# Kernel tuning notes

Hardware: AMD Instinct MI355X
Metric: run time of the kernel (lower is better)

Reference implementation:

```python
import jax, jax.numpy as jnp
import numpy as np

B, C, H, W = 64, 256, 48, 48
NH = 8          # num_heads
DH = C // NH    # per-head dim = 32
DFF = 2 * C     # FFN hidden = 512 (hard-coded d_ffn=feature_dim*2)
M = 64          # base_class_num
EPS_NORM = 1e-5
EPS_LN = 1e-5


def setup_inputs() -> dict:
    key = jax.random.key(0)
    ks = jax.random.split(key, 12)
    s = 0.02
    return {
        "feature": jax.random.normal(ks[0], (B, C, H, W), jnp.float32),
        "base_class_weight": jax.random.normal(ks[1], (M, C), jnp.float32),
        # 1x1-conv projections (weight [out,in], bias [out])
        "wq": jax.random.normal(ks[2], (C, C), jnp.float32) * s,
        "bq": jnp.zeros((C,), jnp.float32),
        "wk": jax.random.normal(ks[3], (C, C), jnp.float32) * s,
        "bk": jnp.zeros((C,), jnp.float32),
        "wv": jax.random.normal(ks[4], (C, C), jnp.float32) * s,
        "bv": jnp.zeros((C,), jnp.float32),
        "wm": jax.random.normal(ks[5], (C, C), jnp.float32) * s,
        "bm": jnp.zeros((C,), jnp.float32),
        # FFN_MLP
        "w1": jax.random.normal(ks[6], (DFF, C), jnp.float32) * s,
        "b1": jnp.zeros((DFF,), jnp.float32),
        "w2": jax.random.normal(ks[7], (C, DFF), jnp.float32) * s,
        "b2": jnp.zeros((C,), jnp.float32),
        "gamma": jnp.ones((C,), jnp.float32),
        "beta": jnp.zeros((C,), jnp.float32),
    }


def reference(feature, base_class_weight, wq, bq, wk, bk, wv, bv, wm, bm,
              w1, b1, w2, b2, gamma, beta):
    b, c, h, w = feature.shape
    n = h * w
    feat_cn = feature.reshape(b, c, n)                 # [B,c,N]  (q input, channel-first)
    feat_nc = feat_cn.transpose(0, 2, 1)               # [B,N,c]  ('feature' var in torch)
    kv_cm = jnp.broadcast_to(base_class_weight.T[None], (b, c, M))  # [B,c,M]

    # 1x1-conv projections then split channels as [dim, heads] (dim outer, per torch view)
    qp = (jnp.einsum('oc,bcn->bon', wq, feat_cn) + bq[None, :, None]).reshape(b, DH, NH, n)
    kp = (jnp.einsum('oc,bcm->bom', wk, kv_cm) + bk[None, :, None]).reshape(b, DH, NH, M)
    vp = (jnp.einsum('oc,bcm->bom', wv, kv_cm) + bv[None, :, None]).reshape(b, DH, NH, M)

    scores = jnp.einsum('bdhn,bdhm->bhnm', qp, kp) / jnp.sqrt(jnp.float32(DH))
    prob = jax.nn.softmax(scores, axis=-1)             # [B,H,N,M]
    x = jnp.einsum('bhnm,bdhm->bdhn', prob, vp)        # [B,dim,H,N]
    merged = jnp.einsum('oc,bcn->bon', wm, x.reshape(b, c, n)) + bm[None, :, None]  # [B,c,N]

    # SFTA cosine re-weighting
    aligned = merged.transpose(0, 2, 1)                # [B,N,c]
    an = aligned / (jnp.linalg.norm(aligned, axis=-1, keepdims=True) + EPS_NORM)
    fn = feat_nc / (jnp.linalg.norm(feat_nc, axis=-1, keepdims=True) + EPS_NORM)
    cos = jnp.sum(an * fn, axis=-1)                    # [B,N]
    out = feat_nc * (cos + 1.0)[:, :, None]            # [B,N,c]

    # FFN_MLP (dropout = identity in eval) + residual + LayerNorm
    h1 = jax.nn.relu(jnp.einsum('bnc,fc->bnf', out, w1) + b1)
    src2 = jnp.einsum('bnf,cf->bnc', h1, w2) + b2
    src = out + src2
    mu = jnp.mean(src, axis=-1, keepdims=True)
    var = jnp.mean(jnp.square(src - mu), axis=-1, keepdims=True)
    src = (src - mu) / jnp.sqrt(var + EPS_LN) * gamma + beta

    return src.transpose(0, 2, 1).reshape(b, c, h, w)
```

## Files before the change

kernel.cpp:

```cpp
#include <hip/hip_runtime.h>

#define Bc   64
#define Cc   256
#define Nn   2304
#define DFFf 512
#define Mm   64
#define NTILE 64
#define NTB   36

typedef __bf16 bf16_t;
typedef __bf16 bf16x8 __attribute__((ext_vector_type(8)));
typedef __bf16 bf16x4 __attribute__((ext_vector_type(4)));
typedef float  f32x4  __attribute__((ext_vector_type(4)));

__device__ __forceinline__ bf16_t cvt(float f) { return (bf16_t)f; }

__device__ __forceinline__ f32x4 mfma16(bf16x8 a, bf16x8 b, f32x4 c) {
    return __builtin_amdgcn_mfma_f32_16x16x32_bf16(a, b, c, 0, 0, 0);
}

__global__ void kv_kernel(const float* __restrict__ wk, const float* __restrict__ bk,
                          const float* __restrict__ wv, const float* __restrict__ bv,
                          const float* __restrict__ bcw,
                          float* __restrict__ Kout, float* __restrict__ Vout) {
    int c = blockIdx.x;
    int m = threadIdx.x;
    const float* wkr = wk + c * Cc;
    const float* wvr = wv + c * Cc;
    const float* br  = bcw + m * Cc;
    float aK = 0.f, aV = 0.f;
    #pragma unroll 8
    for (int i = 0; i < Cc; ++i) {
        float bcv = br[i];
        aK = fmaf(wkr[i], bcv, aK);
        aV = fmaf(wvr[i], bcv, aV);
    }
    Kout[c * Mm + m] = aK + bk[c];
    Vout[c * Mm + m] = aV + bv[c];
}

__global__ void pack_kernel(const float* __restrict__ wq, const float* __restrict__ bq,
                            const float* __restrict__ wm, const float* __restrict__ w1,
                            const float* __restrict__ w2,
                            const float* __restrict__ Kf32, const float* __restrict__ Vf32,
                            bf16_t* __restrict__ wqf, bf16_t* __restrict__ wmf,
                            bf16_t* __restrict__ w1f, bf16_t* __restrict__ w2f,
// ... 19 lines not shown
        int c = (k & 31) * 8 + (k >> 5);
        wmf[e] = cvt(wm[o * 256 + c]);
    } else if (idx < 262144) {
        int e = idx - 131072;
        int j = e & 7, lane = (e >> 3) & 63, rs = e >> 9;
        int ks = rs & 7, rt = rs >> 3;
        w1f[e] = cvt(w1[(rt * 16 + (lane & 15)) * 256 + ks * 32 + (lane >> 4) * 8 + j]);
    } else if (idx < 393216) {
        int e = idx - 262144;
        int j = e & 7, lane = (e >> 3) & 63, rs = e >> 9;
        int ks = rs & 15, rt = rs >> 4;
        w2f[e] = cvt(w2[(rt * 16 + (lane & 15)) * 512 + ks * 32 + (lane >> 4) * 8 + j]);
    } else if (idx < 409600) {
        int e = idx - 393216;
        int j = e & 7, lane = (e >> 3) & 63, hm = e >> 9;
        int mt = hm & 3, h = hm >> 2;
        int lid = lane & 15;
        int d = (lane >> 4) * 8 + j;
        int m = 32 * (mt >> 1) + 4 * (mt & 1) + 8 * (lid >> 2) + (lid & 3);
        Kf[e] = cvt(Kf32[(d * 8 + h) * 64 + m]);
    } else if (idx < 425984) {
        int e = idx - 409600;
        int j = e & 7, lane = (e >> 3) & 63, x = e >> 9;
        int ks = x & 1, rt = (x >> 1) & 1, h = x >> 2;
        int d = rt * 16 + (lane & 15), m = ks * 32 + (lane >> 4) * 8 + j;
        Vf[e] = cvt(Vf32[(d * 8 + h) * 64 + m]);
    } else if (idx < 426240) {
        int op = idx - 425984;
        int c = (op & 31) * 8 + (op >> 5);
        bqp[op] = bq[c];
    }
}

__global__ __launch_bounds__(512, 4) void sfta_mfma(
    const float* __restrict__ feat,
    const bf16_t* __restrict__ wqf, const float* __restrict__ bqp,
    const bf16_t* __restrict__ wmf, const float* __restrict__ bm,
    const bf16_t* __restrict__ w1f, const float* __restrict__ b1,
    const bf16_t* __restrict__ w2f, const float* __restrict__ b2,
    const bf16_t* __restrict__ Kf,  const bf16_t* __restrict__ Vf,
    const float* __restrict__ gam,  const float* __restrict__ bet,
    float* __restrict__ out) {
    __shared__ __align__(16) bf16_t sFeat[64 * 264];
    __shared__ __align__(16) bf16_t sQX[64 * 264];
    __shared__ float sRed[3][8][64];

    const int t    = threadIdx.x;
    const int wid  = t >> 6;
    const int lane = t & 63;
    const int quad = lane >> 4;
    const int lid  = lane & 15;
    const int b    = blockIdx.y;
    const int n0   = blockIdx.x * NTILE;
    const size_t baseF = (size_t)b * Cc * Nn + n0;

    {
        int cb = t >> 4;
        int nb = (t & 15) * 4;
        #pragma unroll
        for (int i = 0; i < 8; ++i) {
            int c = i * 32 + cb;
            const float4 f4 = *(const float4*)(feat + baseF + (size_t)c * Nn + nb);
            sFeat[(nb + 0) * 264 + c] = cvt(f4.x);
            sFeat[(nb + 1) * 264 + c] = cvt(f4.y);
            sFeat[(nb + 2) * 264 + c] = cvt(f4.z);
            sFeat[(nb + 3) * 264 + c] = cvt(f4.w);
        }
    }
    __syncthreads();

    bf16x8 bq[4];
    {
        f32x4 qacc[2][4];
        #pragma unroll
        for (int rtl = 0; rtl < 2; ++rtl)
            #pragma unroll
            for (int nt = 0; nt < 4; ++nt) qacc[rtl][nt] = (f32x4){0.f, 0.f, 0.f, 0.f};
        #pragma unroll
        for (int ks = 0; ks < 8; ++ks) {
            bf16x8 bfr[4];
            #pragma unroll
            for (int nt = 0; nt < 4; ++nt)
                bfr[nt] = *(const bf16x8*)(sFeat + (nt * 16 + lid) * 264 + ks * 32 + quad * 8);
            #pragma unroll
            for (int rtl = 0; rtl < 2; ++rtl) {
                bf16x8 a = *(const bf16x8*)(wqf + (((wid * 2 + rtl) * 8 + ks) * 64 + lane) * 8);
                #pragma unroll
                for (int nt = 0; nt < 4; ++nt) qacc[rtl][nt] = mfma16(a, bfr[nt], qacc[rtl][nt]);
            }
        }
        const float4 qbA = *(const float4*)(bqp + wid * 32 + quad * 8);
        const float4 qbB = *(const float4*)(bqp + wid * 32 + quad * 8 + 4);
        #pragma unroll
        for (int g = 0; g < 4; ++g) {
            bq[g][0] = cvt(qacc[0][g][0] + qbA.x);
            bq[g][1] = cvt(qacc[0][g][1] + qbA.y);
            bq[g][2] = cvt(qacc[0][g][2] + qbA.z);
            bq[g][3] = cvt(qacc[0][g][3] + qbA.w);
            bq[g][4] = cvt(qacc[1][g][0] + qbB.x);
            bq[g][5] = cvt(qacc[1][g][1] + qbB.y);
            bq[g][6] = cvt(qacc[1][g][2] + qbB.z);
            bq[g][7] = cvt(qacc[1][g][3] + qbB.w);
        }
    }

    {
        bf16x8 kb[4], va[4];
        #pragma unroll
        for (int mt = 0; mt < 4; ++mt)
            kb[mt] = *(const bf16x8*)(Kf + ((wid * 4 + mt) * 64 + lane) * 8);
        #pragma unroll
        for (int rv = 0; rv < 4; ++rv)
            va[rv] = *(const bf16x8*)(Vf + ((wid * 4 + rv) * 64 + lane) * 8);
        const float scl2 = 0.17677669529663687f * 1.4426950408889634f;
        #pragma unroll 1
        for (int g = 0; g < 4; ++g) {
            f32x4 sc[4];
            #pragma unroll
            for (int mt = 0; mt < 4; ++mt) {
                f32x4 z = {0.f, 0.f, 0.f, 0.f};
                sc[mt] = mfma16(kb[mt], bq[g], z);
            }
            float f[16];
            #pragma unroll
            for (int mt = 0; mt < 4; ++mt)
                #pragma unroll
                for (int r = 0; r < 4; ++r) f[mt * 4 + r] = sc[mt][r] * scl2;
            float mx = f[0];
            #pragma unroll
            for (int i = 1; i < 16; ++i) mx = fmaxf(mx, f[i]);
            mx = fmaxf(mx, __shfl_xor(mx, 16));
            mx = fmaxf(mx, __shfl_xor(mx, 32));
            float s = 0.f;
            #pragma unroll
            for (int i = 0; i < 16; ++i) { f[i] = exp2f(f[i] - mx); s += f[i]; }
            s += __shfl_xor(s, 16);
            s += __shfl_xor(s, 32);
            float inv = 1.f / s;
            bf16x8 bp[2];
            #pragma unroll
            for (int ks = 0; ks < 2; ++ks)
                #pragma unroll
                for (int jj = 0; jj < 8; ++jj)
                    bp[ks][jj] = cvt(f[(2 * ks + (jj >> 2)) * 4 + (jj & 3)] * inv);
            #pragma unroll
            for (int rv = 0; rv < 2; ++rv) {
                f32x4 x = {0.f, 0.f, 0.f, 0.f};
                x = mfma16(va[rv * 2 + 0], bp[0], x);
                x = mfma16(va[rv * 2 + 1], bp[1], x);
                bf16x4 o;
                #pragma unroll
                for (int r = 0; r < 4; ++r) o[r] = cvt(x[r]);
                *(bf16x4*)(sQX + (g * 16 + lid) * 264 + wid * 32 + rv * 16 + quad * 4) = o;
            }
        }
    }
    __syncthreads();

    f32x4 acc2[2][4];
    float pmf[4], pmm[4], pff[4];
    {
        #pragma unroll
        for (int rtl = 0; rtl < 2; ++rtl)
            #pragma unroll
            for (int nt = 0; nt < 4; ++nt) acc2[rtl][nt] = (f32x4){0.f, 0.f, 0.f, 0.f};
        #pragma unroll
        for (int ks = 0; ks < 8; ++ks) {
            bf16x8 bx[4];
            #pragma unroll
            for (int nt = 0; nt < 4; ++nt)
                bx[nt] = *(const bf16x8*)(sQX + (nt * 16 + lid) * 264 + ks * 32 + quad * 8);
            #pragma unroll
            for (int rtl = 0; rtl < 2; ++rtl) {
                bf16x8 a = *(const bf16x8*)(wmf + (((wid * 2 + rtl) * 8 + ks) * 64 + lane) * 8);
                #pragma unroll
                for (int nt = 0; nt < 4; ++nt) acc2[rtl][nt] = mfma16(a, bx[nt], acc2[rtl][nt]);
            }
        }
        float4 bmv[2];
        bmv[0] = *(const float4*)(bm + (wid * 2 + 0) * 16 + quad * 4);
        bmv[1] = *(const float4*)(bm + (wid * 2 + 1) * 16 + quad * 4);
        #pragma unroll
        for (int nt = 0; nt < 4; ++nt) { pmf[nt] = 0.f; pmm[nt] = 0.f; pff[nt] = 0.f; }
        #pragma unroll
        for (int rtl = 0; rtl < 2; ++rtl) {
            int ob = (wid * 2 + rtl) * 16 + quad * 4;
            #pragma unroll
            for (int nt = 0; nt < 4; ++nt) {
                bf16x4 f4 = *(const bf16x4*)(sFeat + (nt * 16 + lid) * 264 + ob);
                #pragma unroll
                for (int r = 0; r < 4; ++r) {
                    float m = acc2[rtl][nt][r] + bmv[rtl][r];
                    float f = (float)f4[r];
                    pmf[nt] = fmaf(m, f, pmf[nt]);
                    pmm[nt] = fmaf(m, m, pmm[nt]);
                    pff[nt] = fmaf(f, f, pff[nt]);
                }
            }
        }
    }
    #pragma unroll
    for (int nt = 0; nt < 4; ++nt) {
        pmf[nt] += __shfl_xor(pmf[nt], 16); pmf[nt] += __shfl_xor(pmf[nt], 32);
        pmm[nt] += __shfl_xor(pmm[nt], 16); pmm[nt] += __shfl_xor(pmm[nt], 32);
        pff[nt] += __shfl_xor(pff[nt], 16); pff[nt] += __shfl_xor(pff[nt], 32);
    }
    if (lane < 16) {
        #pragma unroll
        for (int nt = 0; nt < 4; ++nt) {
            sRed[0][wid][nt * 16 + lane] = pmf[nt];
            sRed[1][wid][nt * 16 + lane] = pmm[nt];
            sRed[2][wid][nt * 16 + lane] = pff[nt];
        }
    }
    __syncthreads();

    {
        int row = wid * 8 + (lane >> 3);
        int c0  = (lane & 7) * 32;
        float smf = 0.f, smm = 0.f, sff = 0.f;
        #pragma unroll
        for (int k = 0; k < 8; ++k) {
            smf += sRed[0][k][row];
            smm += sRed[1][k][row];
            sff += sRed[2][k][row];
        }
        float scale = smf / ((sqrtf(smm) + 1e-5f) * (sqrtf(sff) + 1e-5f)) + 1.f;
        bf16_t* frow = sFeat + row * 264 + c0;
        #pragma unroll
        for (int i = 0; i < 4; ++i) {
            bf16x8* pp = (bf16x8*)(frow + i * 8);
            bf16x8 v = *pp;
            #pragma unroll
            for (int e = 0; e < 8; ++e) v[e] = cvt((float)v[e] * scale);
            *pp = v;
        }
    }
    __syncthreads();

    #pragma unroll
    for (int rtl = 0; rtl < 2; ++rtl)
        #pragma unroll
        for (int nt = 0; nt < 4; ++nt) acc2[rtl][nt] = (f32x4){0.f, 0.f, 0.f, 0.f};
    #pragma unroll 1
    for (int c = 0; c < 2; ++c) {
        f32x4 a1[2][4];
        #pragma unroll
        for (int rtl = 0; rtl < 2; ++rtl)
            #pragma unroll
            for (int nt = 0; nt < 4; ++nt) a1[rtl][nt] = (f32x4){0.f, 0.f, 0.f, 0.f};
        #pragma unroll
        for (int ks = 0; ks < 8; ++ks) {
            bf16x8 bfr[4];
            #pragma unroll
            for (int nt = 0; nt < 4; ++nt)
                bfr[nt] = *(const bf16x8*)(sFeat + (nt * 16 + lid) * 264 + ks * 32 + quad * 8);
            #pragma unroll
            for (int rtl = 0; rtl < 2; ++rtl) {
                int rt1 = c * 16 + wid * 2 + rtl;
                bf16x8 a = *(const bf16x8*)(w1f + ((rt1 * 8 + ks) * 64 + lane) * 8);
                #pragma unroll
                for (int nt = 0; nt < 4; ++nt) a1[rtl][nt] = mfma16(a, bfr[nt], a1[rtl][nt]);
            }
        }
        #pragma unroll
        for (int rtl = 0; rtl < 2; ++rtl) {
            int rt1 = c * 16 + wid * 2 + rtl;
            const float4 b1v = *(const float4*)(b1 + rt1 * 16 + quad * 4);
            int fl = (wid * 2 + rtl) * 16 + quad * 4;
            #pragma unroll
            for (int nt = 0; nt < 4; ++nt) {
                bf16x4 o;
                o[0] = cvt(fmaxf(a1[rtl][nt][0] + b1v.x, 0.f));
                o[1] = cvt(fmaxf(a1[rtl][nt][1] + b1v.y, 0.f));
                o[2] = cvt(fmaxf(a1[rtl][nt][2] + b1v.z, 0.f));
                o[3] = cvt(fmaxf(a1[rtl][nt][3] + b1v.w, 0.f));
                *(bf16x4*)(sQX + (nt * 16 + lid) * 264 + fl) = o;
            }
        }
        __syncthreads();
        #pragma unroll
        for (int kk = 0; kk < 8; ++kk) {
            bf16x8 bh[4];
            #pragma unroll
            for (int nt = 0; nt < 4; ++nt)
                bh[nt] = *(const bf16x8*)(sQX + (nt * 16 + lid) * 264 + kk * 32 + quad * 8);
            #pragma unroll
            for (int rtl = 0; rtl < 2; ++rtl) {
                bf16x8 a = *(const bf16x8*)(w2f + (((wid * 2 + rtl) * 16 + c * 8 + kk) * 64 + lane) * 8);
                #pragma unroll
                for (int nt = 0; nt < 4; ++nt) acc2[rtl][nt] = mfma16(a, bh[nt], acc2[rtl][nt]);
            }
        }
        __syncthreads();
    }

    float ps[4] = {0.f, 0.f, 0.f, 0.f}, pq[4] = {0.f, 0.f, 0.f, 0.f};
    {
        float4 b2v[2];
        b2v[0] = *(const float4*)(b2 + (wid * 2 + 0) * 16 + quad * 4);
        b2v[1] = *(const float4*)(b2 + (wid * 2 + 1) * 16 + quad * 4);
        #pragma unroll
        for (int rtl = 0; rtl < 2; ++rtl) {
            int ob = (wid * 2 + rtl) * 16 + quad * 4;
            #pragma unroll
            for (int nt = 0; nt < 4; ++nt) {
                bf16x4 f4 = *(const bf16x4*)(sFeat + (nt * 16 + lid) * 264 + ob);
                #pragma unroll
                for (int r = 0; r < 4; ++r) {
                    float v = acc2[rtl][nt][r] + ((const float*)&b2v[rtl])[r] + (float)f4[r];
                    acc2[rtl][nt][r] = v;
                    ps[nt] += v;
                    pq[nt] = fmaf(v, v, pq[nt]);
                }
            }
        }
    }
    #pragma unroll
    for (int nt = 0; nt < 4; ++nt) {
        ps[nt] += __shfl_xor(ps[nt], 16); ps[nt] += __shfl_xor(ps[nt], 32);
        pq[nt] += __shfl_xor(pq[nt], 16); pq[nt] += __shfl_xor(pq[nt], 32);
    }
    if (lane < 16) {
        #pragma unroll
        for (int nt = 0; nt < 4; ++nt) {
            sRed[0][wid][nt * 16 + lane] = ps[nt];
            sRed[1][wid][nt * 16 + lane] = pq[nt];
        }
    }
    __syncthreads();

    float* op = out + baseF;
    float4 gv[2], bv[2];
    gv[0] = *(const float4*)(gam + (wid * 2 + 0) * 16 + quad * 4);
    gv[1] = *(const float4*)(gam + (wid * 2 + 1) * 16 + quad * 4);
    bv[0] = *(const float4*)(bet + (wid * 2 + 0) * 16 + quad * 4);
    bv[1] = *(const float4*)(bet + (wid * 2 + 1) * 16 + quad * 4);
    #pragma unroll
    for (int nt = 0; nt < 4; ++nt) {
        int row = nt * 16 + lid;
        float s = 0.f, q = 0.f;
        #pragma unroll
        for (int k = 0; k < 8; ++k) { s += sRed[0][k][row]; q += sRed[1][k][row]; }
        float mu   = s * (1.f / 256.f);
        float rstd = rsqrtf(q * (1.f / 256.f) - mu * mu + 1e-5f);
        #pragma unroll
        for (int rtl = 0; rtl < 2; ++rtl) {
            int ob = (wid * 2 + rtl) * 16 + quad * 4;
            #pragma unroll
            for (int r = 0; r < 4; ++r) {
                float y = (acc2[rtl][nt][r] - mu) * rstd * ((const float*)&gv[rtl])[r]
                          + ((const float*)&bv[rtl])[r];
                op[(size_t)(ob + r) * Nn + row] = y;
            }
        }
    }
}

extern "C" void kernel_launch(void* const* d_in, const int* in_sizes, int n_in,
                              void* d_out, int out_size, void* d_ws, size_t ws_size,
                              hipStream_t stream) {
    const float* feature = (const float*)d_in[0];
    const float* bcw     = (const float*)d_in[1];
    const float* wq = (const float*)d_in[2];  const float* bq = (const float*)d_in[3];
    const float* wk = (const float*)d_in[4];  const float* bk = (const float*)d_in[5];
    const float* wv = (const float*)d_in[6];  const float* bv = (const float*)d_in[7];
    const float* wm = (const float*)d_in[8];  const float* bm = (const float*)d_in[9];
    const float* w1 = (const float*)d_in[10]; const float* b1 = (const float*)d_in[11];
    const float* w2 = (const float*)d_in[12]; const float* b2 = (const float*)d_in[13];
    const float* gm = (const float*)d_in[14]; const float* bt = (const float*)d_in[15];

    float*  Kf32 = (float*)d_ws;
    float*  Vf32 = Kf32 + 16384;
    bf16_t* wqf  = (bf16_t*)(Vf32 + 16384);
    bf16_t* wmf  = wqf + 65536;
    bf16_t* w1f  = wmf + 65536;
    bf16_t* w2f  = w1f + 131072;
    bf16_t* Kf   = w2f + 131072;
    bf16_t* Vf   = Kf + 16384;
    float*  bqp  = (float*)(Vf + 16384);

    float* op = (float*)d_out;

    hipLaunchKernelGGL(kv_kernel, dim3(Cc), dim3(Mm), 0, stream,
                       wk, bk, wv, bv, bcw, Kf32, Vf32);
    hipLaunchKernelGGL(pack_kernel, dim3((426240 + 255) / 256), dim3(256), 0, stream,
                       wq, bq, wm, w1, w2, Kf32, Vf32,
                       wqf, wmf, w1f, w2f, Kf, Vf, bqp);
    hipLaunchKernelGGL(sfta_mfma, dim3(NTB, Bc), dim3(512), 0, stream,
                       feature, wqf, bqp, wmf, bm, w1f, b1, w2f, b2,
                       Kf, Vf, gm, bt, op);
}
```

Before: 488.7 us.

## Double block to 1024 threads with one 16-row tile per wave

The fused kernel now runs 16 waves per block instead of 8. Each wave owns a single 16-row output tile rather than two, and attention is split so that each head is shared by two waves. Because of that split, Q is staged through shared memory with an extra barrier instead of staying in registers. The reduction buffers are transposed so partial sums can be read with vector loads, and LayerNorm statistics are combined with cross-lane shuffles. The aim is to halve per-thread register and MFMA work to raise occupancy and latency hiding, at the cost of repeated B-fragment LDS loads per wave and an extra synchronisation.

```diff
diff --git a/kernel.cpp b/kernel.cpp
--- a/kernel.cpp
+++ b/kernel.cpp
@@ -12,6 +12,7 @@
 typedef __bf16 bf16x8 __attribute__((ext_vector_type(8)));
 typedef __bf16 bf16x4 __attribute__((ext_vector_type(4)));
 typedef float  f32x4  __attribute__((ext_vector_type(4)));
+typedef float  f32x2  __attribute__((ext_vector_type(2)));
 
 __device__ __forceinline__ bf16_t cvt(float f) { return (bf16_t)f; }
 
@@ -97,7 +98,7 @@
     }
 }
 
-__global__ __launch_bounds__(512, 4) void sfta_mfma(
+__global__ __launch_bounds__(1024, 8) void sfta_mfma(
     const float* __restrict__ feat,
     const bf16_t* __restrict__ wqf, const float* __restrict__ bqp,
     const bf16_t* __restrict__ wmf, const float* __restrict__ bm,
@@ -108,23 +109,26 @@
     float* __restrict__ out) {
     __shared__ __align__(16) bf16_t sFeat[64 * 264];
     __shared__ __align__(16) bf16_t sQX[64 * 264];
-    __shared__ float sRed[3][8][64];
+    __shared__ float sRed[3][64][18];
 
     const int t    = threadIdx.x;
     const int wid  = t >> 6;
     const int lane = t & 63;
     const int quad = lane >> 4;
     const int lid  = lane & 15;
+    const int h    = wid >> 1;
+    const int rtl  = wid & 1;
     const int b    = blockIdx.y;
     const int n0   = blockIdx.x * NTILE;
     const size_t baseF = (size_t)b * Cc * Nn + n0;
 
     {
-        int cb = t >> 4;
-        int nb = (t & 15) * 4;
-        #pragma unroll
-        for (int i = 0; i < 8; ++i) {
-            int c = i * 32 + cb;
+        int c_lo = t & 15;
+        int nb   = ((t >> 4) & 15) * 4;
+        int c_hi = t >> 8;
+        #pragma unroll
+        for (int i = 0; i < 4; ++i) {
+            int c = c_hi * 64 + i * 16 + c_lo;
             const float4 f4 = *(const float4*)(feat + baseF + (size_t)c * Nn + nb);
             sFeat[(nb + 0) * 264 + c] = cvt(f4.x);
             sFeat[(nb + 1) * 264 + c] = cvt(f4.y);
@@ -134,57 +138,50 @@
     }
     __syncthreads();
 
-    bf16x8 bq[4];
-    {
-        f32x4 qacc[2][4];
-        #pragma unroll
-        for (int rtl = 0; rtl < 2; ++rtl)
-            #pragma unroll
-            for (int nt = 0; nt < 4; ++nt) qacc[rtl][nt] = (f32x4){0.f, 0.f, 0.f, 0.f};
+    {
+        f32x4 qacc[4];
+        #pragma unroll
+        for (int nt = 0; nt < 4; ++nt) qacc[nt] = (f32x4){0.f, 0.f, 0.f, 0.f};
         #pragma unroll
         for (int ks = 0; ks < 8; ++ks) {
-            bf16x8 bfr[4];
-            #pragma unroll
-            for (int nt = 0; nt < 4; ++nt)
-                bfr[nt] = *(const bf16x8*)(sFeat + (nt * 16 + lid) * 264 + ks * 32 + quad * 8);
-            #pragma unroll
-            for (int rtl = 0; rtl < 2; ++rtl) {
-                bf16x8 a = *(const bf16x8*)(wqf + (((wid * 2 + rtl) * 8 + ks) * 64 + lane) * 8);
-                #pragma unroll
-                for (int nt = 0; nt < 4; ++nt) qacc[rtl][nt] = mfma16(a, bfr[nt], qacc[rtl][nt]);
-            }
-        }
-        const float4 qbA = *(const float4*)(bqp + wid * 32 + quad * 8);
-        const float4 qbB = *(const float4*)(bqp + wid * 32 + quad * 8 + 4);
-        #pragma unroll
-        for (int g = 0; g < 4; ++g) {
-            bq[g][0] = cvt(qacc[0][g][0] + qbA.x);
-            bq[g][1] = cvt(qacc[0][g][1] + qbA.y);
-            bq[g][2] = cvt(qacc[0][g][2] + qbA.z);
-            bq[g][3] = cvt(qacc[0][g][3] + qbA.w);
-            bq[g][4] = cvt(qacc[1][g][0] + qbB.x);
-            bq[g][5] = cvt(qacc[1][g][1] + qbB.y);
-            bq[g][6] = cvt(qacc[1][g][2] + qbB.z);
-            bq[g][7] = cvt(qacc[1][g][3] + qbB.w);
-        }
-    }
+            bf16x8 a = *(const bf16x8*)(wqf + ((wid * 8 + ks) * 64 + lane) * 8);
+            #pragma unroll
+            for (int nt = 0; nt < 4; ++nt) {
+                bf16x8 bfr = *(const bf16x8*)(sFeat + (nt * 16 + lid) * 264 + ks * 32 + quad * 8);
+                qacc[nt] = mfma16(a, bfr, qacc[nt]);
+            }
+        }
+        const float4 qb = *(const float4*)(bqp + h * 32 + quad * 8 + rtl * 4);
+        #pragma unroll
+        for (int nt = 0; nt < 4; ++nt) {
+            bf16x4 o;
+            o[0] = cvt(qacc[nt][0] + qb.x);
+            o[1] = cvt(qacc[nt][1] + qb.y);
+            o[2] = cvt(qacc[nt][2] + qb.z);
+            o[3] = cvt(qacc[nt][3] + qb.w);
+            *(bf16x4*)(sQX + (nt * 16 + lid) * 264 + h * 32 + quad * 8 + rtl * 4) = o;
+        }
+    }
+    __syncthreads();
 
     {
         bf16x8 kb[4], va[4];
         #pragma unroll
         for (int mt = 0; mt < 4; ++mt)
-            kb[mt] = *(const bf16x8*)(Kf + ((wid * 4 + mt) * 64 + lane) * 8);
+            kb[mt] = *(const bf16x8*)(Kf + ((h * 4 + mt) * 64 + lane) * 8);
         #pragma unroll
         for (int rv = 0; rv < 4; ++rv)
-            va[rv] = *(const bf16x8*)(Vf + ((wid * 4 + rv) * 64 + lane) * 8);
+            va[rv] = *(const bf16x8*)(Vf + ((h * 4 + rv) * 64 + lane) * 8);
         const float scl2 = 0.17677669529663687f * 1.4426950408889634f;
         #pragma unroll 1
-        for (int g = 0; g < 4; ++g) {
+        for (int u = 0; u < 2; ++u) {
+            int g = rtl * 2 + u;
+            bf16x8 aq = *(const bf16x8*)(sQX + (g * 16 + lid) * 264 + h * 32 + quad * 8);
             f32x4 sc[4];
             #pragma unroll
             for (int mt = 0; mt < 4; ++mt) {
                 f32x4 z = {0.f, 0.f, 0.f, 0.f};
-                sc[mt] = mfma16(kb[mt], bq[g], z);
+                sc[mt] = mfma16(kb[mt], aq, z);
             }
             float f[16];
             #pragma unroll
@@ -216,51 +213,39 @@
                 bf16x4 o;
                 #pragma unroll
                 for (int r = 0; r < 4; ++r) o[r] = cvt(x[r]);
-                *(bf16x4*)(sQX + (g * 16 + lid) * 264 + wid * 32 + rv * 16 + quad * 4) = o;
-            }
-        }
-    }
-    __syncthreads();
-
-    f32x4 acc2[2][4];
+                *(bf16x4*)(sQX + (g * 16 + lid) * 264 + h * 32 + rv * 16 + quad * 4) = o;
+            }
+        }
+    }
+    __syncthreads();
+
     float pmf[4], pmm[4], pff[4];
     {
-        #pragma unroll
-        for (int rtl = 0; rtl < 2; ++rtl)
-            #pragma unroll
-            for (int nt = 0; nt < 4; ++nt) acc2[rtl][nt] = (f32x4){0.f, 0.f, 0.f, 0.f};
+        f32x4 acc[4];
+        #pragma unroll
+        for (int nt = 0; nt < 4; ++nt) acc[nt] = (f32x4){0.f, 0.f, 0.f, 0.f};
         #pragma unroll
         for (int ks = 0; ks < 8; ++ks) {
-            bf16x8 bx[4];
-            #pragma unroll
-            for (int nt = 0; nt < 4; ++nt)
-                bx[nt] = *(const bf16x8*)(sQX + (nt * 16 + lid) * 264 + ks * 32 + quad * 8);
-            #pragma unroll
-            for (int rtl = 0; rtl < 2; ++rtl) {
-                bf16x8 a = *(const bf16x8*)(wmf + (((wid * 2 + rtl) * 8 + ks) * 64 + lane) * 8);
-                #pragma unroll
-                for (int nt = 0; nt < 4; ++nt) acc2[rtl][nt] = mfma16(a, bx[nt], acc2[rtl][nt]);
-            }
-        }
-        float4 bmv[2];
-        bmv[0] = *(const float4*)(bm + (wid * 2 + 0) * 16 + quad * 4);
-        bmv[1] = *(const float4*)(bm + (wid * 2 + 1) * 16 + quad * 4);
+            bf16x8 a = *(const bf16x8*)(wmf + ((wid * 8 + ks) * 64 + lane) * 8);
+            #pragma unroll
+            for (int nt = 0; nt < 4; ++nt) {
+                bf16x8 bx = *(const bf16x8*)(sQX + (nt * 16 + lid) * 264 + ks * 32 + quad * 8);
+                acc[nt] = mfma16(a, bx, acc[nt]);
+            }
+        }
+        const float4 bmv = *(const float4*)(bm + wid * 16 + quad * 4);
         #pragma unroll
         for (int nt = 0; nt < 4; ++nt) { pmf[nt] = 0.f; pmm[nt] = 0.f; pff[nt] = 0.f; }
         #pragma unroll
-        for (int rtl = 0; rtl < 2; ++rtl) {
-            int ob = (wid * 2 + rtl) * 16 + quad * 4;
-            #pragma unroll
-            for (int nt = 0; nt < 4; ++nt) {
-                bf16x4 f4 = *(const bf16x4*)(sFeat + (nt * 16 + lid) * 264 + ob);
-                #pragma unroll
-                for (int r = 0; r < 4; ++r) {
-                    float m = acc2[rtl][nt][r] + bmv[rtl][r];
-                    float f = (float)f4[r];
-                    pmf[nt] = fmaf(m, f, pmf[nt]);
-                    pmm[nt] = fmaf(m, m, pmm[nt]);
-                    pff[nt] = fmaf(f, f, pff[nt]);
-                }
+        for (int nt = 0; nt < 4; ++nt) {
+            bf16x4 f4 = *(const bf16x4*)(sFeat + (nt * 16 + lid) * 264 + wid * 16 + quad * 4);
+            #pragma unroll
+            for (int r = 0; r < 4; ++r) {
+                float m = acc[nt][r] + ((const float*)&bmv)[r];
+                float f = (float)f4[r];
+                pmf[nt] = fmaf(m, f, pmf[nt]);
+                pmm[nt] = fmaf(m, m, pmm[nt]);
+                pff[nt] = fmaf(f, f, pff[nt]);
             }
         }
     }
@@ -273,27 +258,29 @@
     if (lane < 16) {
         #pragma unroll
         for (int nt = 0; nt < 4; ++nt) {
-            sRed[0][wid][nt * 16 + lane] = pmf[nt];
-            sRed[1][wid][nt * 16 + lane] = pmm[nt];
-            sRed[2][wid][nt * 16 + lane] = pff[nt];
-        }
-    }
-    __syncthreads();
-
-    {
-        int row = wid * 8 + (lane >> 3);
-        int c0  = (lane & 7) * 32;
+            sRed[0][nt * 16 + lane][wid] = pmf[nt];
+            sRed[1][nt * 16 + lane][wid] = pmm[nt];
+            sRed[2][nt * 16 + lane][wid] = pff[nt];
+        }
+    }
+    __syncthreads();
+
+    {
+        int row = wid * 4 + quad;
         float smf = 0.f, smm = 0.f, sff = 0.f;
         #pragma unroll
-        for (int k = 0; k < 8; ++k) {
-            smf += sRed[0][k][row];
-            smm += sRed[1][k][row];
-            sff += sRed[2][k][row];
+        for (int k2 = 0; k2 < 8; ++k2) {
+            f32x2 a0 = *(const f32x2*)(&sRed[0][row][k2 * 2]);
+            f32x2 a1 = *(const f32x2*)(&sRed[1][row][k2 * 2]);
+            f32x2 a2 = *(const f32x2*)(&sRed[2][row][k2 * 2]);
+            smf += a0[0] + a0[1];
+            smm += a1[0] + a1[1];
+            sff += a2[0] + a2[1];
         }
         float scale = smf / ((sqrtf(smm) + 1e-5f) * (sqrtf(sff) + 1e-5f)) + 1.f;
-        bf16_t* frow = sFeat + row * 264 + c0;
-        #pragma unroll
-        for (int i = 0; i < 4; ++i) {
+        bf16_t* frow = sFeat + row * 264 + lid * 16;
+        #pragma unroll
+        for (int i = 0; i < 2; ++i) {
             bf16x8* pp = (bf16x8*)(frow + i * 8);
             bf16x8 v = *pp;
             #pragma unroll
@@ -303,58 +290,42 @@
     }
     __syncthreads();
 
+    f32x4 acc2[4];
     #pragma unroll
-    for (int rtl = 0; rtl < 2; ++rtl)
-        #pragma unroll
-        for (int nt = 0; nt < 4; ++nt) acc2[rtl][nt] = (f32x4){0.f, 0.f, 0.f, 0.f};
+    for (int nt = 0; nt < 4; ++nt) acc2[nt] = (f32x4){0.f, 0.f, 0.f, 0.f};
     #pragma unroll 1
     for (int c = 0; c < 2; ++c) {
-        f32x4 a1[2][4];
-        #pragma unroll
-        for (int rtl = 0; rtl < 2; ++rtl)
-            #pragma unroll
-            for (int nt = 0; nt < 4; ++nt) a1[rtl][nt] = (f32x4){0.f, 0.f, 0.f, 0.f};
+        int rt1 = c * 16 + wid;
+        f32x4 a1[4];
+        #pragma unroll
+        for (int nt = 0; nt < 4; ++nt) a1[nt] = (f32x4){0.f, 0.f, 0.f, 0.f};
         #pragma unroll
         for (int ks = 0; ks < 8; ++ks) {
-            bf16x8 bfr[4];
-            #pragma unroll
-            for (int nt = 0; nt < 4; ++nt)
-                bfr[nt] = *(const bf16x8*)(sFeat + (nt * 16 + lid) * 264 + ks * 32 + quad * 8);
-            #pragma unroll
-            for (int rtl = 0; rtl < 2; ++rtl) {
-                int rt1 = c * 16 + wid * 2 + rtl;
-                bf16x8 a = *(const bf16x8*)(w1f + ((rt1 * 8 + ks) * 64 + lane) * 8);
-                #pragma unroll
-                for (int nt = 0; nt < 4; ++nt) a1[rtl][nt] = mfma16(a, bfr[nt], a1[rtl][nt]);
-            }
-        }
-        #pragma unroll
-        for (int rtl = 0; rtl < 2; ++rtl) {
-            int rt1 = c * 16 + wid * 2 + rtl;
-            const float4 b1v = *(const float4*)(b1 + rt1 * 16 + quad * 4);
-            int fl = (wid * 2 + rtl) * 16 + quad * 4;
+            bf16x8 a = *(const bf16x8*)(w1f + ((rt1 * 8 + ks) * 64 + lane) * 8);
             #pragma unroll
             for (int nt = 0; nt < 4; ++nt) {
-                bf16x4 o;
-                o[0] = cvt(fmaxf(a1[rtl][nt][0] + b1v.x, 0.f));
-                o[1] = cvt(fmaxf(a1[rtl][nt][1] + b1v.y, 0.f));
-                o[2] = cvt(fmaxf(a1[rtl][nt][2] + b1v.z, 0.f));
-                o[3] = cvt(fmaxf(a1[rtl][nt][3] + b1v.w, 0.f));
-                *(bf16x4*)(sQX + (nt * 16 + lid) * 264 + fl) = o;
-            }
+                bf16x8 bfr = *(const bf16x8*)(sFeat + (nt * 16 + lid) * 264 + ks * 32 + quad * 8);
+                a1[nt] = mfma16(a, bfr, a1[nt]);
+            }
+        }
+        const float4 b1v = *(const float4*)(b1 + rt1 * 16 + quad * 4);
+        #pragma unroll
+        for (int nt = 0; nt < 4; ++nt) {
+            bf16x4 o;
+            o[0] = cvt(fmaxf(a1[nt][0] + b1v.x, 0.f));
+            o[1] = cvt(fmaxf(a1[nt][1] + b1v.y, 0.f));
+            o[2] = cvt(fmaxf(a1[nt][2] + b1v.z, 0.f));
+            o[3] = cvt(fmaxf(a1[nt][3] + b1v.w, 0.f));
+            *(bf16x4*)(sQX + (nt * 16 + lid) * 264 + wid * 16 + quad * 4) = o;
         }
         __syncthreads();
         #pragma unroll
         for (int kk = 0; kk < 8; ++kk) {
-            bf16x8 bh[4];
-            #pragma unroll
-            for (int nt = 0; nt < 4; ++nt)
-                bh[nt] = *(const bf16x8*)(sQX + (nt * 16 + lid) * 264 + kk * 32 + quad * 8);
-            #pragma unroll
-            for (int rtl = 0; rtl < 2; ++rtl) {
-                bf16x8 a = *(const bf16x8*)(w2f + (((wid * 2 + rtl) * 16 + c * 8 + kk) * 64 + lane) * 8);
-                #pragma unroll
-                for (int nt = 0; nt < 4; ++nt) acc2[rtl][nt] = mfma16(a, bh[nt], acc2[rtl][nt]);
+            bf16x8 a = *(const bf16x8*)(w2f + ((wid * 16 + c * 8 + kk) * 64 + lane) * 8);
+            #pragma unroll
+            for (int nt = 0; nt < 4; ++nt) {
+                bf16x8 bh = *(const bf16x8*)(sQX + (nt * 16 + lid) * 264 + kk * 32 + quad * 8);
+                acc2[nt] = mfma16(a, bh, acc2[nt]);
             }
         }
         __syncthreads();
@@ -362,22 +333,16 @@
 
     float ps[4] = {0.f, 0.f, 0.f, 0.f}, pq[4] = {0.f, 0.f, 0.f, 0.f};
     {
-        float4 b2v[2];
-        b2v[0] = *(const float4*)(b2 + (wid * 2 + 0) * 16 + quad * 4);
-        b2v[1] = *(const float4*)(b2 + (wid * 2 + 1) * 16 + quad * 4);
-        #pragma unroll
-        for (int rtl = 0; rtl < 2; ++rtl) {
-            int ob = (wid * 2 + rtl) * 16 + quad * 4;
-            #pragma unroll
-            for (int nt = 0; nt < 4; ++nt) {
-                bf16x4 f4 = *(const bf16x4*)(sFeat + (nt * 16 + lid) * 264 + ob);
-                #pragma unroll
-                for (int r = 0; r < 4; ++r) {
-                    float v = acc2[rtl][nt][r] + ((const float*)&b2v[rtl])[r] + (float)f4[r];
-                    acc2[rtl][nt][r] = v;
-                    ps[nt] += v;
-                    pq[nt] = fmaf(v, v, pq[nt]);
-                }
+        const float4 b2v = *(const float4*)(b2 + wid * 16 + quad * 4);
+        #pragma unroll
+        for (int nt = 0; nt < 4; ++nt) {
+            bf16x4 f4 = *(const bf16x4*)(sFeat + (nt * 16 + lid) * 264 + wid * 16 + quad * 4);
+            #pragma unroll
+            for (int r = 0; r < 4; ++r) {
+                float v = acc2[nt][r] + ((const float*)&b2v)[r] + (float)f4[r];
+                acc2[nt][r] = v;
+                ps[nt] += v;
+                pq[nt] = fmaf(v, v, pq[nt]);
             }
         }
     }
@@ -389,35 +354,36 @@
     if (lane < 16) {
         #pragma unroll
         for (int nt = 0; nt < 4; ++nt) {
-            sRed[0][wid][nt * 16 + lane] = ps[nt];
-            sRed[1][wid][nt * 16 + lane] = pq[nt];
+            sRed[0][nt * 16 + lane][wid] = ps[nt];
+            sRed[1][nt * 16 + lane][wid] = pq[nt];
         }
     }
     __syncthreads();
 
     float* op = out + baseF;
-    float4 gv[2], bv[2];
-    gv[0] = *(const float4*)(gam + (wid * 2 + 0) * 16 + quad * 4);
-    gv[1] = *(const float4*)(gam + (wid * 2 + 1) * 16 + quad * 4);
-    bv[0] = *(const float4*)(bet + (wid * 2 + 0) * 16 + quad * 4);
-    bv[1] = *(const float4*)(bet + (wid * 2 + 1) * 16 + quad * 4);
+    const float4 gv = *(const float4*)(gam + wid * 16 + quad * 4);
+    const float4 bv = *(const float4*)(bet + wid * 16 + quad * 4);
     #pragma unroll
     for (int nt = 0; nt < 4; ++nt) {
         int row = nt * 16 + lid;
         float s = 0.f, q = 0.f;
         #pragma unroll
-        for (int k = 0; k < 8; ++k) { s += sRed[0][k][row]; q += sRed[1][k][row]; }
+        for (int k2 = 0; k2 < 2; ++k2) {
+            f32x2 a0 = *(const f32x2*)(&sRed[0][row][quad * 4 + k2 * 2]);
+            f32x2 a1 = *(const f32x2*)(&sRed[1][row][quad * 4 + k2 * 2]);
+            s += a0[0] + a0[1];
+            q += a1[0] + a1[1];
+        }
+        s += __shfl_xor(s, 16); s += __shfl_xor(s, 32);
+        q += __shfl_xor(q, 16); q += __shfl_xor(q, 32);
         float mu   = s * (1.f / 256.f);
         float rstd = rsqrtf(q * (1.f / 256.f) - mu * mu + 1e-5f);
-        #pragma unroll
-        for (int rtl = 0; rtl < 2; ++rtl) {
-            int ob = (wid * 2 + rtl) * 16 + quad * 4;
-            #pragma unroll
-            for (int r = 0; r < 4; ++r) {
-                float y = (acc2[rtl][nt][r] - mu) * rstd * ((const float*)&gv[rtl])[r]
-                          + ((const float*)&bv[rtl])[r];
-                op[(size_t)(ob + r) * Nn + row] = y;
-            }
+        int ob = wid * 16 + quad * 4;
+        #pragma unroll
+        for (int r = 0; r < 4; ++r) {
+            float y = (acc2[nt][r] - mu) * rstd * ((const float*)&gv)[r]
+                      + ((const float*)&bv)[r];
+            op[(size_t)(ob + r) * Nn + row] = y;
         }
     }
 }
@@ -452,7 +418,7 @@
     hipLaunchKernelGGL(pack_kernel, dim3((426240 + 255) / 256), dim3(256), 0, stream,
                        wq, bq, wm, w1, w2, Kf32, Vf32,
                        wqf, wmf, w1f, w2f, Kf, Vf, bqp);
-    hipLaunchKernelGGL(sfta_mfma, dim3(NTB, Bc), dim3(512), 0, stream,
+    hipLaunchKernelGGL(sfta_mfma, dim3(NTB, Bc), dim3(1024), 0, stream,
                        feature, wqf, bqp, wmf, bm, w1f, b1, w2f, b2,
                        Kf, Vf, gm, bt, op);
 }
```

Result: faster. 455.7 us (-6.8%).

## Halve token tile to 32, raise occupancy, and simplify softmax normalization

Applied to the files above, without the earlier changes.

Cuts the per-block token tile from 64 to 32, doubling the grid and raising the occupancy hint from 4 to 6 blocks per SM. Shared buffers and all MFMA loops shrink to match. The feature load becomes per-thread column gathers written as 16-byte vector stores, and the reduction buffers are transposed. The softmax drops the max subtraction and applies the 1/sum after the PV MFMA. This trades weight reuse per block (weights are re-read by twice as many blocks) for more parallelism, and risks exp overflow if scores ever grow large.

```diff
diff --git a/kernel.cpp b/kernel.cpp
--- a/kernel.cpp
+++ b/kernel.cpp
@@ -5,8 +5,8 @@
 #define Nn   2304
 #define DFFf 512
 #define Mm   64
-#define NTILE 64
-#define NTB   36
+#define NTILE 32
+#define NTB   72
 
 typedef __bf16 bf16_t;
 typedef __bf16 bf16x8 __attribute__((ext_vector_type(8)));
@@ -97,7 +97,7 @@
     }
 }
 
-__global__ __launch_bounds__(512, 4) void sfta_mfma(
+__global__ __launch_bounds__(512, 6) void sfta_mfma(
     const float* __restrict__ feat,
     const bf16_t* __restrict__ wqf, const float* __restrict__ bqp,
     const bf16_t* __restrict__ wmf, const float* __restrict__ bm,
@@ -106,9 +106,9 @@
     const bf16_t* __restrict__ Kf,  const bf16_t* __restrict__ Vf,
     const float* __restrict__ gam,  const float* __restrict__ bet,
     float* __restrict__ out) {
-    __shared__ __align__(16) bf16_t sFeat[64 * 264];
-    __shared__ __align__(16) bf16_t sQX[64 * 264];
-    __shared__ float sRed[3][8][64];
+    __shared__ __align__(16) bf16_t sFeat[32 * 264];
+    __shared__ __align__(16) bf16_t sQX[32 * 264];
+    __shared__ float sRed[3][32][12];
 
     const int t    = threadIdx.x;
     const int wid  = t >> 6;
@@ -120,52 +120,52 @@
     const size_t baseF = (size_t)b * Cc * Nn + n0;
 
     {
-        int cb = t >> 4;
-        int nb = (t & 15) * 4;
-        #pragma unroll
-        for (int i = 0; i < 8; ++i) {
-            int c = i * 32 + cb;
-            const float4 f4 = *(const float4*)(feat + baseF + (size_t)c * Nn + nb);
-            sFeat[(nb + 0) * 264 + c] = cvt(f4.x);
-            sFeat[(nb + 1) * 264 + c] = cvt(f4.y);
-            sFeat[(nb + 2) * 264 + c] = cvt(f4.z);
-            sFeat[(nb + 3) * 264 + c] = cvt(f4.w);
-        }
+        int nl = t & 31;
+        int c0 = (t >> 5) * 16;
+        const float* gp = feat + baseF + (size_t)c0 * Nn + nl;
+        float v[16];
+        #pragma unroll
+        for (int j = 0; j < 16; ++j) v[j] = gp[(size_t)j * Nn];
+        bf16x8 lo, hi;
+        #pragma unroll
+        for (int j = 0; j < 8; ++j) { lo[j] = cvt(v[j]); hi[j] = cvt(v[8 + j]); }
+        *(bf16x8*)(sFeat + nl * 264 + c0)     = lo;
+        *(bf16x8*)(sFeat + nl * 264 + c0 + 8) = hi;
     }
     __syncthreads();
 
-    bf16x8 bq[4];
+    bf16x8 bq[2];
     {
-        f32x4 qacc[2][4];
+        f32x4 qacc[2][2];
         #pragma unroll
         for (int rtl = 0; rtl < 2; ++rtl)
             #pragma unroll
-            for (int nt = 0; nt < 4; ++nt) qacc[rtl][nt] = (f32x4){0.f, 0.f, 0.f, 0.f};
+            for (int nt = 0; nt < 2; ++nt) qacc[rtl][nt] = (f32x4){0.f, 0.f, 0.f, 0.f};
         #pragma unroll
         for (int ks = 0; ks < 8; ++ks) {
-            bf16x8 bfr[4];
-            #pragma unroll
-            for (int nt = 0; nt < 4; ++nt)
+            bf16x8 bfr[2];
+            #pragma unroll
+            for (int nt = 0; nt < 2; ++nt)
                 bfr[nt] = *(const bf16x8*)(sFeat + (nt * 16 + lid) * 264 + ks * 32 + quad * 8);
             #pragma unroll
             for (int rtl = 0; rtl < 2; ++rtl) {
                 bf16x8 a = *(const bf16x8*)(wqf + (((wid * 2 + rtl) * 8 + ks) * 64 + lane) * 8);
                 #pragma unroll
-                for (int nt = 0; nt < 4; ++nt) qacc[rtl][nt] = mfma16(a, bfr[nt], qacc[rtl][nt]);
+                for (int nt = 0; nt < 2; ++nt) qacc[rtl][nt] = mfma16(a, bfr[nt], qacc[rtl][nt]);
             }
         }
         const float4 qbA = *(const float4*)(bqp + wid * 32 + quad * 8);
         const float4 qbB = *(const float4*)(bqp + wid * 32 + quad * 8 + 4);
         #pragma unroll
-        for (int g = 0; g < 4; ++g) {
-            bq[g][0] = cvt(qacc[0][g][0] + qbA.x);
-            bq[g][1] = cvt(qacc[0][g][1] + qbA.y);
-            bq[g][2] = cvt(qacc[0][g][2] + qbA.z);
-            bq[g][3] = cvt(qacc[0][g][3] + qbA.w);
-            bq[g][4] = cvt(qacc[1][g][0] + qbB.x);
-            bq[g][5] = cvt(qacc[1][g][1] + qbB.y);
-            bq[g][6] = cvt(qacc[1][g][2] + qbB.z);
-            bq[g][7] = cvt(qacc[1][g][3] + qbB.w);
+        for (int nt = 0; nt < 2; ++nt) {
+            bq[nt][0] = cvt(qacc[0][nt][0] + qbA.x);
+            bq[nt][1] = cvt(qacc[0][nt][1] + qbA.y);
+            bq[nt][2] = cvt(qacc[0][nt][2] + qbA.z);
+            bq[nt][3] = cvt(qacc[0][nt][3] + qbA.w);
+            bq[nt][4] = cvt(qacc[1][nt][0] + qbB.x);
+            bq[nt][5] = cvt(qacc[1][nt][1] + qbB.y);
+            bq[nt][6] = cvt(qacc[1][nt][2] + qbB.z);
+            bq[nt][7] = cvt(qacc[1][nt][3] + qbB.w);
         }
     }
 
@@ -179,35 +179,23 @@
             va[rv] = *(const bf16x8*)(Vf + ((wid * 4 + rv) * 64 + lane) * 8);
         const float scl2 = 0.17677669529663687f * 1.4426950408889634f;
         #pragma unroll 1
-        for (int g = 0; g < 4; ++g) {
-            f32x4 sc[4];
+        for (int g = 0; g < 2; ++g) {
+            float s = 0.f;
+            bf16x8 bp[2];
             #pragma unroll
             for (int mt = 0; mt < 4; ++mt) {
                 f32x4 z = {0.f, 0.f, 0.f, 0.f};
-                sc[mt] = mfma16(kb[mt], bq[g], z);
-            }
-            float f[16];
-            #pragma unroll
-            for (int mt = 0; mt < 4; ++mt)
-                #pragma unroll
-                for (int r = 0; r < 4; ++r) f[mt * 4 + r] = sc[mt][r] * scl2;
-            float mx = f[0];
-            #pragma unroll
-            for (int i = 1; i < 16; ++i) mx = fmaxf(mx, f[i]);
-            mx = fmaxf(mx, __shfl_xor(mx, 16));
-            mx = fmaxf(mx, __shfl_xor(mx, 32));
-            float s = 0.f;
-            #pragma unroll
-            for (int i = 0; i < 16; ++i) { f[i] = exp2f(f[i] - mx); s += f[i]; }
+                f32x4 sc = mfma16(kb[mt], bq[g], z);
+                #pragma unroll
+                for (int r = 0; r < 4; ++r) {
+                    float e = exp2f(sc[r] * scl2);
+                    s += e;
+                    bp[mt >> 1][(mt & 1) * 4 + r] = cvt(e);
+                }
+            }
             s += __shfl_xor(s, 16);
             s += __shfl_xor(s, 32);
             float inv = 1.f / s;
-            bf16x8 bp[2];
-            #pragma unroll
-            for (int ks = 0; ks < 2; ++ks)
-                #pragma unroll
-                for (int jj = 0; jj < 8; ++jj)
-                    bp[ks][jj] = cvt(f[(2 * ks + (jj >> 2)) * 4 + (jj & 3)] * inv);
             #pragma unroll
             for (int rv = 0; rv < 2; ++rv) {
                 f32x4 x = {0.f, 0.f, 0.f, 0.f};
@@ -215,47 +203,45 @@
                 x = mfma16(va[rv * 2 + 1], bp[1], x);
                 bf16x4 o;
                 #pragma unroll
-                for (int r = 0; r < 4; ++r) o[r] = cvt(x[r]);
+                for (int r = 0; r < 4; ++r) o[r] = cvt(x[r] * inv);
                 *(bf16x4*)(sQX + (g * 16 + lid) * 264 + wid * 32 + rv * 16 + quad * 4) = o;
             }
         }
     }
     __syncthreads();
 
-    f32x4 acc2[2][4];
-    float pmf[4], pmm[4], pff[4];
+    float pmf[2], pmm[2], pff[2];
     {
+        f32x4 acc[2][2];
         #pragma unroll
         for (int rtl = 0; rtl < 2; ++rtl)
             #pragma unroll
-            for (int nt = 0; nt < 4; ++nt) acc2[rtl][nt] = (f32x4){0.f, 0.f, 0.f, 0.f};
+            for (int nt = 0; nt < 2; ++nt) acc[rtl][nt] = (f32x4){0.f, 0.f, 0.f, 0.f};
         #pragma unroll
         for (int ks = 0; ks < 8; ++ks) {
-            bf16x8 bx[4];
-            #pragma unroll
-            for (int nt = 0; nt < 4; ++nt)
+            bf16x8 bx[2];
+            #pragma unroll
+            for (int nt = 0; nt < 2; ++nt)
                 bx[nt] = *(const bf16x8*)(sQX + (nt * 16 + lid) * 264 + ks * 32 + quad * 8);
             #pragma unroll
             for (int rtl = 0; rtl < 2; ++rtl) {
                 bf16x8 a = *(const bf16x8*)(wmf + (((wid * 2 + rtl) * 8 + ks) * 64 + lane) * 8);
                 #pragma unroll
-                for (int nt = 0; nt < 4; ++nt) acc2[rtl][nt] = mfma16(a, bx[nt], acc2[rtl][nt]);
-            }
-        }
-        float4 bmv[2];
-        bmv[0] = *(const float4*)(bm + (wid * 2 + 0) * 16 + quad * 4);
-        bmv[1] = *(const float4*)(bm + (wid * 2 + 1) * 16 + quad * 4);
-        #pragma unroll
-        for (int nt = 0; nt < 4; ++nt) { pmf[nt] = 0.f; pmm[nt] = 0.f; pff[nt] = 0.f; }
+                for (int nt = 0; nt < 2; ++nt) acc[rtl][nt] = mfma16(a, bx[nt], acc[rtl][nt]);
+            }
+        }
+        #pragma unroll
+        for (int nt = 0; nt < 2; ++nt) { pmf[nt] = 0.f; pmm[nt] = 0.f; pff[nt] = 0.f; }
         #pragma unroll
         for (int rtl = 0; rtl < 2; ++rtl) {
             int ob = (wid * 2 + rtl) * 16 + quad * 4;
-            #pragma unroll
-            for (int nt = 0; nt < 4; ++nt) {
+            const float4 bmv = *(const float4*)(bm + ob);
+            #pragma unroll
+            for (int nt = 0; nt < 2; ++nt) {
                 bf16x4 f4 = *(const bf16x4*)(sFeat + (nt * 16 + lid) * 264 + ob);
                 #pragma unroll
                 for (int r = 0; r < 4; ++r) {
-                    float m = acc2[rtl][nt][r] + bmv[rtl][r];
+                    float m = acc[rtl][nt][r] + ((const float*)&bmv)[r];
                     float f = (float)f4[r];
                     pmf[nt] = fmaf(m, f, pmf[nt]);
                     pmm[nt] = fmaf(m, m, pmm[nt]);
@@ -265,35 +251,34 @@
         }
     }
     #pragma unroll
-    for (int nt = 0; nt < 4; ++nt) {
+    for (int nt = 0; nt < 2; ++nt) {
         pmf[nt] += __shfl_xor(pmf[nt], 16); pmf[nt] += __shfl_xor(pmf[nt], 32);
         pmm[nt] += __shfl_xor(pmm[nt], 16); pmm[nt] += __shfl_xor(pmm[nt], 32);
         pff[nt] += __shfl_xor(pff[nt], 16); pff[nt] += __shfl_xor(pff[nt], 32);
     }
     if (lane < 16) {
         #pragma unroll
-        for (int nt = 0; nt < 4; ++nt) {
-            sRed[0][wid][nt * 16 + lane] = pmf[nt];
-            sRed[1][wid][nt * 16 + lane] = pmm[nt];
-            sRed[2][wid][nt * 16 + lane] = pff[nt];
+        for (int nt = 0; nt < 2; ++nt) {
+            sRed[0][nt * 16 + lane][wid] = pmf[nt];
+            sRed[1][nt * 16 + lane][wid] = pmm[nt];
+            sRed[2][nt * 16 + lane][wid] = pff[nt];
         }
     }
     __syncthreads();
 
     {
-        int row = wid * 8 + (lane >> 3);
-        int c0  = (lane & 7) * 32;
+        int row = wid * 4 + quad;
         float smf = 0.f, smm = 0.f, sff = 0.f;
         #pragma unroll
         for (int k = 0; k < 8; ++k) {
-            smf += sRed[0][k][row];
-            smm += sRed[1][k][row];
-            sff += sRed[2][k][row];
+            smf += sRed[0][row][k];
+            smm += sRed[1][row][k];
+            sff += sRed[2][row][k];
         }
         float scale = smf / ((sqrtf(smm) + 1e-5f) * (sqrtf(sff) + 1e-5f)) + 1.f;
-        bf16_t* frow = sFeat + row * 264 + c0;
-        #pragma unroll
-        for (int i = 0; i < 4; ++i) {
+        bf16_t* frow = sFeat + row * 264 + lid * 16;
+        #pragma unroll
+        for (int i = 0; i < 2; ++i) {
             bf16x8* pp = (bf16x8*)(frow + i * 8);
             bf16x8 v = *pp;
             #pragma unroll
@@ -303,119 +288,116 @@
     }
     __syncthreads();
 
+    f32x4 acc2[2][2];
     #pragma unroll
     for (int rtl = 0; rtl < 2; ++rtl)
         #pragma unroll
-        for (int nt = 0; nt < 4; ++nt) acc2[rtl][nt] = (f32x4){0.f, 0.f, 0.f, 0.f};
+        for (int nt = 0; nt < 2; ++nt) acc2[rtl][nt] = (f32x4){0.f, 0.f, 0.f, 0.f};
     #pragma unroll 1
     for (int c = 0; c < 2; ++c) {
-        f32x4 a1[2][4];
-        #pragma unroll
-        for (int rtl = 0; rtl < 2; ++rtl)
-            #pragma unroll
-            for (int nt = 0; nt < 4; ++nt) a1[rtl][nt] = (f32x4){0.f, 0.f, 0.f, 0.f};
-        #pragma unroll
-        for (int ks = 0; ks < 8; ++ks) {
-            bf16x8 bfr[4];
-            #pragma unroll
-            for (int nt = 0; nt < 4; ++nt)
-                bfr[nt] = *(const bf16x8*)(sFeat + (nt * 16 + lid) * 264 + ks * 32 + quad * 8);
+        {
+            f32x4 a1[2][2];
+            #pragma unroll
+            for (int rtl = 0; rtl < 2; ++rtl)
+                #pragma unroll
+                for (int nt = 0; nt < 2; ++nt) a1[rtl][nt] = (f32x4){0.f, 0.f, 0.f, 0.f};
+            #pragma unroll
+            for (int ks = 0; ks < 8; ++ks) {
+                bf16x8 bfr[2];
+                #pragma unroll
+                for (int nt = 0; nt < 2; ++nt)
+                    bfr[nt] = *(const bf16x8*)(sFeat + (nt * 16 + lid) * 264 + ks * 32 + quad * 8);
+                #pragma unroll
+                for (int rtl = 0; rtl < 2; ++rtl) {
+                    int rt1 = c * 16 + wid * 2 + rtl;
+                    bf16x8 a = *(const bf16x8*)(w1f + ((rt1 * 8 + ks) * 64 + lane) * 8);
+                    #pragma unroll
+                    for (int nt = 0; nt < 2; ++nt) a1[rtl][nt] = mfma16(a, bfr[nt], a1[rtl][nt]);
+                }
+            }
             #pragma unroll
             for (int rtl = 0; rtl < 2; ++rtl) {
                 int rt1 = c * 16 + wid * 2 + rtl;
-                bf16x8 a = *(const bf16x8*)(w1f + ((rt1 * 8 + ks) * 64 + lane) * 8);
-                #pragma unroll
-                for (int nt = 0; nt < 4; ++nt) a1[rtl][nt] = mfma16(a, bfr[nt], a1[rtl][nt]);
-            }
-        }
-        #pragma unroll
-        for (int rtl = 0; rtl < 2; ++rtl) {
-            int rt1 = c * 16 + wid * 2 + rtl;
-            const float4 b1v = *(const float4*)(b1 + rt1 * 16 + quad * 4);
-            int fl = (wid * 2 + rtl) * 16 + quad * 4;
-            #pragma unroll
-            for (int nt = 0; nt < 4; ++nt) {
-                bf16x4 o;
-                o[0] = cvt(fmaxf(a1[rtl][nt][0] + b1v.x, 0.f));
-                o[1] = cvt(fmaxf(a1[rtl][nt][1] + b1v.y, 0.f));
-                o[2] = cvt(fmaxf(a1[rtl][nt][2] + b1v.z, 0.f));
-                o[3] = cvt(fmaxf(a1[rtl][nt][3] + b1v.w, 0.f));
-                *(bf16x4*)(sQX + (nt * 16 + lid) * 264 + fl) = o;
+                const float4 b1v = *(const float4*)(b1 + rt1 * 16 + quad * 4);
+                int fl = (wid * 2 + rtl) * 16 + quad * 4;
+                #pragma unroll
+                for (int nt = 0; nt < 2; ++nt) {
+                    bf16x4 o;
+                    o[0] = cvt(fmaxf(a1[rtl][nt][0] + b1v.x, 0.f));
+                    o[1] = cvt(fmaxf(a1[rtl][nt][1] + b1v.y, 0.f));
+                    o[2] = cvt(fmaxf(a1[rtl][nt][2] + b1v.z, 0.f));
+                    o[3] = cvt(fmaxf(a1[rtl][nt][3] + b1v.w, 0.f));
+                    *(bf16x4*)(sQX + (nt * 16 + lid) * 264 + fl) = o;
+                }
             }
         }
         __syncthreads();
         #pragma unroll
         for (int kk = 0; kk < 8; ++kk) {
-            bf16x8 bh[4];
-            #pragma unroll
-            for (int nt = 0; nt < 4; ++nt)
+            bf16x8 bh[2];
+            #pragma unroll
+            for (int nt = 0; nt < 2; ++nt)
                 bh[nt] = *(const bf16x8*)(sQX + (nt * 16 + lid) * 264 + kk * 32 + quad * 8);
             #pragma unroll
             for (int rtl = 0; rtl < 2; ++rtl) {
                 bf16x8 a = *(const bf16x8*)(w2f + (((wid * 2 + rtl) * 16 + c * 8 + kk) * 64 + lane) * 8);
                 #pragma unroll
-                for (int nt = 0; nt < 4; ++nt) acc2[rtl][nt] = mfma16(a, bh[nt], acc2[rtl][nt]);
+                for (int nt = 0; nt < 2; ++nt) acc2[rtl][nt] = mfma16(a, bh[nt], acc2[rtl][nt]);
             }
         }
         __syncthreads();
     }
 
-    float ps[4] = {0.f, 0.f, 0.f, 0.f}, pq[4] = {0.f, 0.f, 0.f, 0.f};
-    {
-        float4 b2v[2];
-        b2v[0] = *(const float4*)(b2 + (wid * 2 + 0) * 16 + quad * 4);
-        b2v[1] = *(const float4*)(b2 + (wid * 2 + 1) * 16 + quad * 4);
+    float ps[2] = {0.f, 0.f}, pq[2] = {0.f, 0.f};
+    #pragma unroll
+    for (int rtl = 0; rtl < 2; ++rtl) {
+        int ob = (wid * 2 + rtl) * 16 + quad * 4;
+        const float4 b2v = *(const float4*)(b2 + ob);
+        #pragma unroll
+        for (int nt = 0; nt < 2; ++nt) {
+            bf16x4 f4 = *(const bf16x4*)(sFeat + (nt * 16 + lid) * 264 + ob);
+            #pragma unroll
+            for (int r = 0; r < 4; ++r) {
+                float v = acc2[rtl][nt][r] + ((const float*)&b2v)[r] + (float)f4[r];
+                acc2[rtl][nt][r] = v;
+                ps[nt] += v;
+                pq[nt] = fmaf(v, v, pq[nt]);
+            }
+        }
+    }
+    #pragma unroll
+    for (int nt = 0; nt < 2; ++nt) {
+        ps[nt] += __shfl_xor(ps[nt], 16); ps[nt] += __shfl_xor(ps[nt], 32);
+        pq[nt] += __shfl_xor(pq[nt], 16); pq[nt] += __shfl_xor(pq[nt], 32);
+    }
+    if (lane < 16) {
+        #pragma unroll
+        for (int nt = 0; nt < 2; ++nt) {
+            sRed[0][nt * 16 + lane][wid] = ps[nt];
+            sRed[1][nt * 16 + lane][wid] = pq[nt];
+        }
+    }
+    __syncthreads();
+
+    float* op = out + baseF;
+    #pragma unroll
+    for (int nt = 0; nt < 2; ++nt) {
+        int row = nt * 16 + lid;
+        float s = sRed[0][row][quad * 2] + sRed[0][row][quad * 2 + 1];
+        float q = sRed[1][row][quad * 2] + sRed[1][row][quad * 2 + 1];
+        s += __shfl_xor(s, 16); s += __shfl_xor(s, 32);
+        q += __shfl_xor(q, 16); q += __shfl_xor(q, 32);
+        float mu   = s * (1.f / 256.f);
+        float rstd = rsqrtf(q * (1.f / 256.f) - mu * mu + 1e-5f);
         #pragma unroll
         for (int rtl = 0; rtl < 2; ++rtl) {
             int ob = (wid * 2 + rtl) * 16 + quad * 4;
-            #pragma unroll
-            for (int nt = 0; nt < 4; ++nt) {
-                bf16x4 f4 = *(const bf16x4*)(sFeat + (nt * 16 + lid) * 264 + ob);
-                #pragma unroll
-                for (int r = 0; r < 4; ++r) {
-                    float v = acc2[rtl][nt][r] + ((const float*)&b2v[rtl])[r] + (float)f4[r];
-                    acc2[rtl][nt][r] = v;
-                    ps[nt] += v;
-                    pq[nt] = fmaf(v, v, pq[nt]);
-                }
-            }
-        }
-    }
-    #pragma unroll
-    for (int nt = 0; nt < 4; ++nt) {
-        ps[nt] += __shfl_xor(ps[nt], 16); ps[nt] += __shfl_xor(ps[nt], 32);
-        pq[nt] += __shfl_xor(pq[nt], 16); pq[nt] += __shfl_xor(pq[nt], 32);
-    }
-    if (lane < 16) {
-        #pragma unroll
-        for (int nt = 0; nt < 4; ++nt) {
-            sRed[0][wid][nt * 16 + lane] = ps[nt];
-            sRed[1][wid][nt * 16 + lane] = pq[nt];
-        }
-    }
-    __syncthreads();
-
-    float* op = out + baseF;
-    float4 gv[2], bv[2];
-    gv[0] = *(const float4*)(gam + (wid * 2 + 0) * 16 + quad * 4);
-    gv[1] = *(const float4*)(gam + (wid * 2 + 1) * 16 + quad * 4);
-    bv[0] = *(const float4*)(bet + (wid * 2 + 0) * 16 + quad * 4);
-    bv[1] = *(const float4*)(bet + (wid * 2 + 1) * 16 + quad * 4);
-    #pragma unroll
-    for (int nt = 0; nt < 4; ++nt) {
-        int row = nt * 16 + lid;
-        float s = 0.f, q = 0.f;
-        #pragma unroll
-        for (int k = 0; k < 8; ++k) { s += sRed[0][k][row]; q += sRed[1][k][row]; }
-        float mu   = s * (1.f / 256.f);
-        float rstd = rsqrtf(q * (1.f / 256.f) - mu * mu + 1e-5f);
-        #pragma unroll
-        for (int rtl = 0; rtl < 2; ++rtl) {
-            int ob = (wid * 2 + rtl) * 16 + quad * 4;
+            const float4 gv = *(const float4*)(gam + ob);
+            const float4 bv = *(const float4*)(bet + ob);
             #pragma unroll
             for (int r = 0; r < 4; ++r) {
-                float y = (acc2[rtl][nt][r] - mu) * rstd * ((const float*)&gv[rtl])[r]
-                          + ((const float*)&bv[rtl])[r];
+                float y = (acc2[rtl][nt][r] - mu) * rstd * ((const float*)&gv)[r]
+                          + ((const float*)&bv)[r];
                 op[(size_t)(ob + r) * Nn + row] = y;
             }
         }
```

New measurement: 468.9 us. -4.1%, faster.
